# Performance work log

Measured on AMD Instinct MI355X. Metric: run time of the kernel, lower is better.

Reference implementation:

```python
import jax, jax.numpy as jnp
import numpy as np

TOP_K = 8
N_EXPERTS = 64
HIDDEN = 4096


def setup_inputs() -> dict:
    key = jax.random.key(0)
    k1, k2 = jax.random.split(key)
    hidden_states = jax.random.normal(k1, (4, 4096, HIDDEN), dtype=jnp.float32)
    # kaiming_uniform_(a=sqrt(5)) on a (64, 4096) weight -> U(-b, b), b = sqrt(6/((1+5)*4096)) = 1/sqrt(4096)
    bound = 1.0 / np.sqrt(HIDDEN)
    weight = jax.random.uniform(k2, (N_EXPERTS, HIDDEN), dtype=jnp.float32,
                                minval=-bound, maxval=bound)
    return {"hidden_states": hidden_states, "weight": weight}


def reference(hidden_states, weight):
    bsz, seq_len, h = hidden_states.shape
    x = hidden_states.reshape(-1, h)                       # [T, H]
    logits = jnp.einsum('th,eh->te', x, weight)            # [T, E]
    scores = jax.nn.softmax(logits, axis=-1)
    topk_weight, topk_idx = jax.lax.top_k(scores, TOP_K)   # [T, K]
    denom = jnp.sum(topk_weight, axis=-1, keepdims=True) + 1e-20
    topk_weight = topk_weight / denom
    topk_weight = topk_weight.reshape(bsz, seq_len, TOP_K)
    topk_idx = topk_idx.reshape(bsz, seq_len, TOP_K)
    # training-time aux loss (seq_aux path): histogram of argmax expert * mean prob
    probs = scores                                         # softmax(logits)
    top1 = jnp.argmax(probs, axis=-1)                      # [T]
    counts = jnp.zeros((N_EXPERTS,), dtype=jnp.float32).at[top1].add(1.0)
    route_prob = jnp.mean(probs, axis=0)                   # [E]
    route_frac = counts / jnp.sum(counts)
    aux_loss = jnp.sum(route_prob * route_frac) * N_EXPERTS
    return topk_idx, topk_weight, aux_loss
```

## Files before the change

### kernel.cpp

```cpp
#include <hip/hip_runtime.h>
#include <hip/hip_bf16.h>

#define TOKS 16384
#define HID  4096
#define NEXP 64
#define EPS  1e-4f

#define WS_FLAGCNT  128
#define WS_FLAGLIST 192
#define WS_BPACK    16576
#define BPK_LO      262144

typedef __attribute__((ext_vector_type(8))) short short8_t;
typedef __attribute__((ext_vector_type(4))) float f32x4;

static __device__ __forceinline__ unsigned short f2bf_rn(float x) {
    unsigned u = __builtin_bit_cast(unsigned, x);
    u = (u + 0x7fffu + ((u >> 16) & 1u)) >> 16;
    return (unsigned short)u;
}
static __device__ __forceinline__ float bf2f(unsigned short h) {
    return __builtin_bit_cast(float, (unsigned)h << 16);
}

__global__ void moe_prep(const float* __restrict__ W, unsigned short* __restrict__ Bpk,
                         float* __restrict__ wsf) {
    const int idx = blockIdx.x * blockDim.x + threadIdx.x;
    if (idx < 192) wsf[idx] = 0.0f;
    if (idx >= NEXP * HID) return;
    const int n = idx >> 12;
    const int k = idx & 4095;
    const float w = W[idx];
    const unsigned short hi = f2bf_rn(w);
    const unsigned short lo = f2bf_rn(w - bf2f(hi));
    const int kt   = k >> 5;
    const int nt   = n >> 4;
    const int lane = (n & 15) | (((k >> 3) & 3) << 4);
    const int j    = k & 7;
    const int dst  = (((kt << 2) + nt) << 9) + (lane << 3) + j;
    Bpk[dst]          = hi;
    Bpk[BPK_LO + dst] = lo;
}

__global__ __launch_bounds__(512, 4)
void moe_fused(const float* __restrict__ X, const unsigned short* __restrict__ Bpk,
               float* __restrict__ out, float* __restrict__ wsf) {
    __shared__ __align__(16) float L[8][16][68];

    const int tid  = threadIdx.x;
    const int lane = tid & 63;
    const int w    = tid >> 6;
    const int tok0 = blockIdx.x * 32;

    const int mrow = lane & 15;
    const int g    = lane >> 4;
    const size_t xoff0 = (size_t)(tok0 + mrow) * HID + ((size_t)w << 9) + (g << 3);
    const size_t xoff1 = xoff0 + (size_t)16 * HID;
    const unsigned short* bb0 = Bpk + (((size_t)w << 4) << 11) + (lane << 3);

    f32x4 acc[2][4];
    #pragma unroll
    for (int mt = 0; mt < 2; ++mt)
        #pragma unroll
        for (int nt = 0; nt < 4; ++nt) acc[mt][nt] = (f32x4){0.f, 0.f, 0.f, 0.f};

    float4 nxa0 = *(const float4*)&X[xoff0];
    float4 nxb0 = *(const float4*)&X[xoff0 + 4];
    float4 nxa1 = *(const float4*)&X[xoff1];
    float4 nxb1 = *(const float4*)&X[xoff1 + 4];

    #pragma unroll 4
    for (int c = 0; c < 16; ++c) {
        const float4 xa0 = nxa0, xb0 = nxb0, xa1 = nxa1, xb1 = nxb1;
        if (c < 15) {
            nxa0 = *(const float4*)&X[xoff0 + ((c + 1) << 5)];
            nxb0 = *(const float4*)&X[xoff0 + ((c + 1) << 5) + 4];
            nxa1 = *(const float4*)&X[xoff1 + ((c + 1) << 5)];
            nxb1 = *(const float4*)&X[xoff1 + ((c + 1) << 5) + 4];
        }
        short8_t ah[2], al[2];
        {
            const float xv0[8] = {xa0.x, xa0.y, xa0.z, xa0.w, xb0.x, xb0.y, xb0.z, xb0.w};
            const float xv1[8] = {xa1.x, xa1.y, xa1.z, xa1.w, xb1.x, xb1.y, xb1.z, xb1.w};
            #pragma unroll
            for (int j = 0; j < 8; ++j) {
                unsigned short hh = f2bf_rn(xv0[j]);
                ah[0][j] = (short)hh;
                al[0][j] = (short)f2bf_rn(xv0[j] - bf2f(hh));
                hh = f2bf_rn(xv1[j]);
                ah[1][j] = (short)hh;
                al[1][j] = (short)f2bf_rn(xv1[j] - bf2f(hh));
            }
        }
        const unsigned short* bb = bb0 + ((size_t)c << 11);
        #pragma unroll
        for (int nt = 0; nt < 4; ++nt) {
            const short8_t bh = *(const short8_t*)(bb + (nt << 9));
            const short8_t bl = *(const short8_t*)(bb + BPK_LO + (nt << 9));
            #pragma unroll
            for (int mt = 0; mt < 2; ++mt) {
                acc[mt][nt] = __builtin_amdgcn_mfma_f32_16x16x32_bf16(ah[mt], bh, acc[mt][nt], 0, 0, 0);
                acc[mt][nt] = __builtin_amdgcn_mfma_f32_16x16x32_bf16(al[mt], bh, acc[mt][nt], 0, 0, 0);
                acc[mt][nt] = __builtin_amdgcn_mfma_f32_16x16x32_bf16(ah[mt], bl, acc[mt][nt], 0, 0, 0);
            }
        }
    }

    float* outIdx = out;
    float* outW   = out + TOKS * 8;
    int* flagcnt  = (int*)wsf + WS_FLAGCNT;
    int* flaglist = (int*)wsf + WS_FLAGLIST;

    float rp = 0.f;
    #pragma unroll
    for (int ph = 0; ph < 2; ++ph) {
        if (ph) __syncthreads();
        #pragma unroll
        for (int nt = 0; nt < 4; ++nt)
            #pragma unroll
            for (int r = 0; r < 4; ++r)
                L[w][(g << 2) + r][(nt << 4) + mrow] = acc[ph][nt][r];
        __syncthreads();

        #pragma unroll
        for (int tt = 0; tt < 2; ++tt) {
            const int tl = (w << 1) + tt;
            const float lg = ((L[0][tl][lane] + L[1][tl][lane]) + (L[2][tl][lane] + L[3][tl][lane]))
                           + ((L[4][tl][lane] + L[5][tl][lane]) + (L[6][tl][lane] + L[7][tl][lane]));

            float v = lg; int idx = lane;
            #pragma unroll
            for (int size = 2; size <= 64; size <<= 1) {
                #pragma unroll
                for (int str = size >> 1; str > 0; str >>= 1) {
                    const float ov = __shfl_xor(v, str, 64);
                    const int   oi = __shfl_xor(idx, str, 64);
                    const bool pb = (ov > v) || (ov == v && oi < idx);
                    const bool keepFirst = ((lane & str) == 0) == ((lane & size) == 0);
                    if (pb == keepFirst) { v = ov; idx = oi; }
                }
            }

            const float m = __shfl(v, 0, 64);
            const float p = __expf(lg - m);
            float s = p;
            #pragma unroll
            for (int o = 32; o; o >>= 1) s += __shfl_xor(s, o, 64);
            const float inv_s = 1.0f / s;
            rp += p * inv_s;

            const float wkv = __expf(v - m) * inv_s;
            float d8 = (lane < 8) ? wkv : 0.f;
            #pragma unroll
            for (int o = 1; o < 8; o <<= 1) d8 += __shfl_xor(d8, o, 64);
            const float invd = 1.0f / (d8 + 1e-20f);
            const float nv = __shfl_down(v, 1, 64);
            const bool flg = __any(lane < 8 && (v - nv) < EPS);

            const int gtok = tok0 + (ph << 4) + tl;
            if (lane < 8) {
                outIdx[(size_t)gtok * 8 + lane] = (float)idx;
                outW[(size_t)gtok * 8 + lane]   = wkv * invd;
            }
            if (lane == 0) {
                atomicAdd(&wsf[NEXP + idx], 1.0f);
                if (flg) {
                    const int pos = atomicAdd(flagcnt, 1);
                    if (pos < TOKS) flaglist[pos] = gtok;
                }
            }
        }
    }
    atomicAdd(&wsf[lane], rp);
}

__global__ __launch_bounds__(256, 2)
void moe_fix(const float* __restrict__ X, const float* __restrict__ W,
             float* __restrict__ out, float* __restrict__ wsf) {
    __shared__ double red[256];
    const int tid = threadIdx.x;
    const int e   = tid & 63;
    const int kc  = tid >> 6;
    const int nf  = min(*((int*)wsf + WS_FLAGCNT), TOKS);
    const int* flaglist = (const int*)wsf + WS_FLAGLIST;
    float* outIdx = out;
    float* outW   = out + TOKS * 8;

    for (int fi = blockIdx.x; fi < nf; fi += gridDim.x) {
        const int tok = flaglist[fi];
        const float* xrow = X + (size_t)tok * HID + kc * 1024;
        const float* wrow = W + (size_t)e  * HID + kc * 1024;
        double part = 0.0;
        for (int j = 0; j < 1024; j += 4) {
            const float4 xv = *(const float4*)(xrow + j);
            const float4 wv = *(const float4*)(wrow + j);
            part = fma((double)xv.x, (double)wv.x, part);
            part = fma((double)xv.y, (double)wv.y, part);
            part = fma((double)xv.z, (double)wv.z, part);
            part = fma((double)xv.w, (double)wv.w, part);
        }
        red[tid] = part;
        __syncthreads();
        if (tid < 64) {
            const double lg = ((red[tid] + red[64 + tid]) + red[128 + tid]) + red[192 + tid];
            const float lgf = (float)lg;
            float m = lgf;
            #pragma unroll
            for (int o = 32; o; o >>= 1) m = fmaxf(m, __shfl_xor(m, o, 64));
            const float p = __expf(lgf - m);
            float s = p;
            #pragma unroll
            for (int o = 32; o; o >>= 1) s += __shfl_xor(s, o, 64);
            const float inv_s = 1.0f / s;

            double v = lg;
            double bw[8]; int ik[8];
            #pragma unroll
            for (int k = 0; k < 8; ++k) {
                double bv = v; int bi = tid;
                #pragma unroll
                for (int o = 32; o; o >>= 1) {
                    const double ov = __shfl_xor(bv, o, 64);
                    const int    oi = __shfl_xor(bi, o, 64);
                    if (ov > bv || (ov == bv && oi < bi)) { bv = ov; bi = oi; }
                }
                bw[k] = bv; ik[k] = bi;
                if (tid == bi) v = -1.0e300;
            }
            float wk[8]; float denom = 1e-20f;
            #pragma unroll
            for (int k = 0; k < 8; ++k) {
                wk[k] = __expf((float)bw[k] - m) * inv_s; denom += wk[k];
            }
            const float invd = 1.0f / denom;
            const size_t base = (size_t)tok * 8;
            const int oldtop = (int)outIdx[base];
            if (tid < 8) {
                outIdx[base + tid] = (float)ik[tid];
                outW[base + tid]   = wk[tid] * invd;
            }
            if (tid == 0 && ik[0] != oldtop) {
                atomicAdd(&wsf[NEXP + oldtop], -1.0f);
                atomicAdd(&wsf[NEXP + ik[0]],  1.0f);
            }
        }
        __syncthreads();
    }
}

__global__ void moe_final(const float* __restrict__ wsf, float* __restrict__ out) {
    const int e = threadIdx.x;
    float v = wsf[e] * wsf[NEXP + e];
    #pragma unroll
    for (int o = 32; o; o >>= 1) v += __shfl_xor(v, o, 64);
    if (e == 0)
        out[2 * TOKS * 8] = v * (64.0f / ((float)TOKS * (float)TOKS));
}

__global__ void moe_init(float* __restrict__ wsf, int n) {
    const int i = blockIdx.x * blockDim.x + threadIdx.x;
    if (i < n) wsf[i] = 0.0f;
}

__global__ void moe_w_cvt(const float* __restrict__ W, double* __restrict__ Wd) {
    const int i = blockIdx.x * blockDim.x + threadIdx.x;
    if (i < NEXP * HID) Wd[i] = (double)W[i];
}

__global__ __launch_bounds__(512, 2)
void moe_mono(const float* __restrict__ X, const double* __restrict__ Wd,
              float* __restrict__ out, float* __restrict__ wsf) {
    __shared__ double xs[64][66];
    __shared__ double L2[64][65];
    const int tid  = threadIdx.x;
    const int lane = tid & 63;
    const int wid  = __builtin_amdgcn_readfirstlane(tid >> 6);
    const int tok0 = blockIdx.x * 64;
    double acc[8] = {0., 0., 0., 0., 0., 0., 0., 0.};
    for (int h0 = 0; h0 < HID; h0 += 64) {
        #pragma unroll
        for (int i = 0; i < 8; ++i) {
            const int li = tid + i * 512;
            xs[li >> 6][li & 63] = (double)X[((size_t)(tok0 + (li >> 6)) << 12) + (h0 + (li & 63))];
        }
        __syncthreads();
        const double* wchunk = Wd + (((size_t)(wid << 3)) << 12) + h0;
        #pragma unroll 2
        for (int hh = 0; hh < 64; hh += 2) {
            const double2 xv = *(const double2*)&xs[lane][hh];
            #pragma unroll
            for (int e = 0; e < 8; ++e) {
                const double* wr = wchunk + (((size_t)e) << 12) + hh;
                acc[e] = fma(xv.x, wr[0], acc[e]);
                acc[e] = fma(xv.y, wr[1], acc[e]);
            }
        }
        __syncthreads();
    }
    #pragma unroll
    for (int e = 0; e < 8; ++e) L2[lane][(wid << 3) + e] = acc[e];
    __syncthreads();
    float* outIdx = out;
    float* outW   = out + (TOKS * 8);
    float rp = 0.0f;
    for (int tt = 0; tt < 8; ++tt) {
        const int t = (wid << 3) + tt;
        const double lg = L2[t][lane];
        const float lgf = (float)lg;
        float m = lgf;
        #pragma unroll
        for (int o = 32; o; o >>= 1) m = fmaxf(m, __shfl_xor(m, o, 64));
        const float p = __expf(lgf - m);
        float s = p;
        #pragma unroll
        for (int o = 32; o; o >>= 1) s += __shfl_xor(s, o, 64);
        const float inv_s = 1.0f / s;
        rp += p * inv_s;
        double v = lg;
        float wk[8]; int ik[8];
        #pragma unroll
        for (int k = 0; k < 8; ++k) {
            double bv = v; int bi = lane;
            #pragma unroll
            for (int o = 32; o; o >>= 1) {
                const double ov = __shfl_xor(bv, o, 64);
                const int    oi = __shfl_xor(bi, o, 64);
                if (ov > bv || (ov == bv && oi < bi)) { bv = ov; bi = oi; }
            }
            wk[k] = __expf((float)bv - m) * inv_s; ik[k] = bi;
            if (lane == bi) v = -1.0e300;
        }
        if (lane == 0) {
            const float denom = (((wk[0]+wk[1])+(wk[2]+wk[3])) +
                                 ((wk[4]+wk[5])+(wk[6]+wk[7]))) + 1e-20f;
            const float invd = 1.0f / denom;
            const size_t base = ((size_t)(tok0 + t)) << 3;
            #pragma unroll
            for (int k = 0; k < 8; ++k) {
                outIdx[base + k] = (float)ik[k];
                outW[base + k]   = wk[k] * invd;
            }
            atomicAdd(&wsf[NEXP + ik[0]], 1.0f);
        }
    }
    atomicAdd(&wsf[lane], rp);
}

extern "C" void kernel_launch(void* const* d_in, const int* in_sizes, int n_in,
                              void* d_out, int out_size, void* d_ws, size_t ws_size,
                              hipStream_t stream) {
    const float* X = (const float*)d_in[0];
    const float* W = (const float*)d_in[1];
    float* out = (float*)d_out;
    float* wsf = (float*)d_ws;

    const size_t need = 4ull * WS_BPACK + 4ull * BPK_LO;

    if (ws_size >= need) {
        unsigned short* Bpk = (unsigned short*)(wsf + WS_BPACK);
        moe_prep<<<(NEXP * HID + 255) / 256, 256, 0, stream>>>(W, Bpk, wsf);
        moe_fused<<<TOKS / 32, 512, 0, stream>>>(X, Bpk, out, wsf);
        moe_fix<<<256, 256, 0, stream>>>(X, W, out, wsf);
        moe_final<<<1, 64, 0, stream>>>(wsf, out);
    } else {
        double* Wd = (double*)d_ws;
        float* wsf2 = (float*)(Wd + NEXP * HID);
        moe_w_cvt<<<(NEXP * HID + 255) / 256, 256, 0, stream>>>(W, Wd);
        moe_init<<<1, 256, 0, stream>>>(wsf2, 128);
        moe_mono<<<TOKS / 64, 512, 0, stream>>>(X, Wd, out, wsf2);
        moe_final<<<1, 64, 0, stream>>>(wsf2, out);
    }
}
```

Before: 210.7 us.

## Interleave hi/lo bf16 weight packing and double-buffer B loads in registers

```diff
diff --git a/kernel.cpp b/kernel.cpp
--- a/kernel.cpp
+++ b/kernel.cpp
@@ -9,7 +9,6 @@
 #define WS_FLAGCNT  128
 #define WS_FLAGLIST 192
 #define WS_BPACK    16576
-#define BPK_LO      262144
 
 typedef __attribute__((ext_vector_type(8))) short short8_t;
 typedef __attribute__((ext_vector_type(4))) float f32x4;
@@ -37,12 +36,12 @@
     const int nt   = n >> 4;
     const int lane = (n & 15) | (((k >> 3) & 3) << 4);
     const int j    = k & 7;
-    const int dst  = (((kt << 2) + nt) << 9) + (lane << 3) + j;
-    Bpk[dst]          = hi;
-    Bpk[BPK_LO + dst] = lo;
-}
-
-__global__ __launch_bounds__(512, 4)
+    const int dst  = (((kt << 2) + nt) << 10) + (lane << 4) + j;
+    Bpk[dst]     = hi;
+    Bpk[dst + 8] = lo;
+}
+
+__global__ __launch_bounds__(512, 2)
 void moe_fused(const float* __restrict__ X, const unsigned short* __restrict__ Bpk,
                float* __restrict__ out, float* __restrict__ wsf) {
     __shared__ __align__(16) float L[8][16][68];
@@ -56,7 +55,7 @@
     const int g    = lane >> 4;
     const size_t xoff0 = (size_t)(tok0 + mrow) * HID + ((size_t)w << 9) + (g << 3);
     const size_t xoff1 = xoff0 + (size_t)16 * HID;
-    const unsigned short* bb0 = Bpk + (((size_t)w << 4) << 11) + (lane << 3);
+    const unsigned short* bb0 = Bpk + ((size_t)w << 16) + (lane << 4);
 
     f32x4 acc[2][4];
     #pragma unroll
@@ -64,19 +63,32 @@
         #pragma unroll
         for (int nt = 0; nt < 4; ++nt) acc[mt][nt] = (f32x4){0.f, 0.f, 0.f, 0.f};
 
+    short8_t bh[2][4], bl[2][4];
     float4 nxa0 = *(const float4*)&X[xoff0];
     float4 nxb0 = *(const float4*)&X[xoff0 + 4];
     float4 nxa1 = *(const float4*)&X[xoff1];
     float4 nxb1 = *(const float4*)&X[xoff1 + 4];
-
-    #pragma unroll 4
+    #pragma unroll
+    for (int nt = 0; nt < 4; ++nt) {
+        bh[0][nt] = *(const short8_t*)(bb0 + (nt << 10));
+        bl[0][nt] = *(const short8_t*)(bb0 + (nt << 10) + 8);
+    }
+
+    #pragma unroll
     for (int c = 0; c < 16; ++c) {
+        const int cur = c & 1, nxt = cur ^ 1;
         const float4 xa0 = nxa0, xb0 = nxb0, xa1 = nxa1, xb1 = nxb1;
         if (c < 15) {
             nxa0 = *(const float4*)&X[xoff0 + ((c + 1) << 5)];
             nxb0 = *(const float4*)&X[xoff0 + ((c + 1) << 5) + 4];
             nxa1 = *(const float4*)&X[xoff1 + ((c + 1) << 5)];
             nxb1 = *(const float4*)&X[xoff1 + ((c + 1) << 5) + 4];
+            const unsigned short* bbn = bb0 + ((size_t)(c + 1) << 12);
+            #pragma unroll
+            for (int nt = 0; nt < 4; ++nt) {
+                bh[nxt][nt] = *(const short8_t*)(bbn + (nt << 10));
+                bl[nxt][nt] = *(const short8_t*)(bbn + (nt << 10) + 8);
+            }
         }
         short8_t ah[2], al[2];
         {
@@ -92,16 +104,13 @@
                 al[1][j] = (short)f2bf_rn(xv1[j] - bf2f(hh));
             }
         }
-        const unsigned short* bb = bb0 + ((size_t)c << 11);
         #pragma unroll
         for (int nt = 0; nt < 4; ++nt) {
-            const short8_t bh = *(const short8_t*)(bb + (nt << 9));
-            const short8_t bl = *(const short8_t*)(bb + BPK_LO + (nt << 9));
             #pragma unroll
             for (int mt = 0; mt < 2; ++mt) {
-                acc[mt][nt] = __builtin_amdgcn_mfma_f32_16x16x32_bf16(ah[mt], bh, acc[mt][nt], 0, 0, 0);
-                acc[mt][nt] = __builtin_amdgcn_mfma_f32_16x16x32_bf16(al[mt], bh, acc[mt][nt], 0, 0, 0);
-                acc[mt][nt] = __builtin_amdgcn_mfma_f32_16x16x32_bf16(ah[mt], bl, acc[mt][nt], 0, 0, 0);
+                acc[mt][nt] = __builtin_amdgcn_mfma_f32_16x16x32_bf16(ah[mt], bh[cur][nt], acc[mt][nt], 0, 0, 0);
+                acc[mt][nt] = __builtin_amdgcn_mfma_f32_16x16x32_bf16(al[mt], bh[cur][nt], acc[mt][nt], 0, 0, 0);
+                acc[mt][nt] = __builtin_amdgcn_mfma_f32_16x16x32_bf16(ah[mt], bl[cur][nt], acc[mt][nt], 0, 0, 0);
             }
         }
     }
@@ -354,7 +363,7 @@
     float* out = (float*)d_out;
     float* wsf = (float*)d_ws;
 
-    const size_t need = 4ull * WS_BPACK + 4ull * BPK_LO;
+    const size_t need = 4ull * WS_BPACK + 2ull * 524288;
 
     if (ws_size >= need) {
         unsigned short* Bpk = (unsigned short*)(wsf + WS_BPACK);
```

Result: slower. 219.7 us (+4.3%).
